# Kernel tuning notes

Measured on AMD Instinct MI355X. Metric: run time of the kernel, lower is better.

The kernel has to match this reference:

```python
import jax, jax.numpy as jnp
import numpy as np
from jax import lax

B, T_ENC, E = 32, 256, 512
A_RNN, D_RNN, P = 1024, 1024, 256
N_MEL, T_DEC = 80, 800
A_DIM, N_FILT, K = 128, 32, 31
PAD = (K - 1) // 2


def setup_inputs() -> dict:
    key = jax.random.key(0)
    ks = jax.random.split(key, 20)
    rn = lambda k, s, sc=0.02: jax.random.normal(k, s, dtype=jnp.float32) * sc
    return {
        "encoder_outputs": jax.random.normal(ks[0], (B, T_ENC, E), dtype=jnp.float32),
        "decoder_inputs": jax.random.normal(ks[1], (B, N_MEL, T_DEC), dtype=jnp.float32),
        "input_lengths": jax.random.randint(ks[2], (B,), 128, T_ENC + 1),
        "prenet_w1": rn(ks[3], (P, N_MEL)),
        "prenet_w2": rn(ks[4], (P, P)),
        "attn_rnn_Wih": rn(ks[5], (4 * A_RNN, P + E)),
        "attn_rnn_Whh": rn(ks[6], (4 * A_RNN, A_RNN)),
        "attn_rnn_bih": jnp.zeros((4 * A_RNN,), jnp.float32),
        "attn_rnn_bhh": jnp.zeros((4 * A_RNN,), jnp.float32),
        "query_W": rn(ks[7], (A_RNN, A_DIM)),
        "memory_W": rn(ks[8], (E, A_DIM)),
        "v_w": rn(ks[9], (A_DIM,)),
        "loc_conv_W": rn(ks[10], (N_FILT, 2, K)),
        "loc_lin_W": rn(ks[11], (N_FILT, A_DIM)),
        "dec_rnn_Wih": rn(ks[12], (4 * D_RNN, A_RNN + E)),
        "dec_rnn_Whh": rn(ks[13], (4 * D_RNN, D_RNN)),
        "dec_rnn_bih": jnp.zeros((4 * D_RNN,), jnp.float32),
        "dec_rnn_bhh": jnp.zeros((4 * D_RNN,), jnp.float32),
        "proj_W": rn(ks[14], (D_RNN + E, N_MEL)),
        "proj_b": jnp.zeros((N_MEL,), jnp.float32),
        "gate_W": rn(ks[15], (D_RNN + E, 1)),
        "gate_b": jnp.zeros((1,), jnp.float32),
    }


def _lstm_cell(xin, h0, c0, Wih, Whh, bih, bhh):
    # PyTorch LSTMCell gate order: i, f, g, o
    g = xin @ Wih.T + bih + h0 @ Whh.T + bhh
    i, f, gg, o = jnp.split(g, 4, axis=-1)
    c = jax.nn.sigmoid(f) * c0 + jax.nn.sigmoid(i) * jnp.tanh(gg)
    return jax.nn.sigmoid(o) * jnp.tanh(c), c


def _forward(encoder_outputs, decoder_inputs, prenet_w1, prenet_w2,
             attn_rnn_Wih, attn_rnn_Whh, attn_rnn_bih, attn_rnn_bhh,
             query_W, memory_W, v_w, loc_conv_W, loc_lin_W,
             dec_rnn_Wih, dec_rnn_Whh, dec_rnn_bih, dec_rnn_bhh,
             proj_W, proj_b, gate_W, gate_b, input_lengths):
    b, t_enc, e = encoder_outputs.shape
    n_mel = decoder_inputs.shape[1]
    dt = encoder_outputs.dtype

    # parse_decoder_inputs + go frame; keep the T_dec frames actually consumed
    x = jnp.transpose(decoder_inputs, (2, 0, 1))               # [T_dec, B, n_mel]
    go = jnp.zeros((1, b, n_mel), dt)
    x = jnp.concatenate([go, x], 0)[:-1]                       # [T_dec, B, n_mel]

    # Prenet: relu->dropout(p=0.5, always on) x2 (deterministic keys)
    k1, k2 = jax.random.split(jax.random.key(42))
    h = jax.nn.relu(jnp.einsum('tbm,pm->tbp', x, prenet_w1))
    h = h * jax.random.bernoulli(k1, 0.5, h.shape) * 2.0
    h = jax.nn.relu(jnp.einsum('tbp,qp->tbq', h, prenet_w2))
    pre = h * jax.random.bernoulli(k2, 0.5, h.shape) * 2.0     # [T_dec, B, P]

    valid = jnp.arange(t_enc)[None, :] < input_lengths[:, None]  # [B, T_enc]
    pmem = jnp.einsum('bte,ea->bta', encoder_outputs, memory_W)  # processed memory

    def step(carry, xstep):
        ah, ac, dh, dc, ctx, aw, awc = carry
        ah, ac = _lstm_cell(jnp.concatenate([xstep, ctx], -1), ah, ac,
                            attn_rnn_Wih, attn_rnn_Whh, attn_rnn_bih, attn_rnn_bhh)
        # location-sensitive attention (LSA)
        loc = jnp.stack([aw, awc], 1)                           # [B, 2, T_enc]
        lf = lax.conv_general_dilated(loc, loc_conv_W, (1,), [(PAD, PAD)],
                                      dimension_numbers=('NCH', 'OIH', 'NCH'))
        lf = jnp.einsum('bft,fa->bta', lf, loc_lin_W)           # [B, T_enc, A_DIM]
        q = ah @ query_W                                        # [B, A_DIM]
        energies = jnp.tanh(q[:, None, :] + lf + pmem) @ v_w    # [B, T_enc]
        energies = jnp.where(valid, energies, jnp.asarray(-1e9, dt))
        aw = jax.nn.softmax(energies, axis=-1)
        awc = awc + aw
        ctx = jnp.einsum('bt,bte->be', aw, encoder_outputs)
        dh, dc = _lstm_cell(jnp.concatenate([ah, ctx], -1), dh, dc,
                            dec_rnn_Wih, dec_rnn_Whh, dec_rnn_bih, dec_rnn_bhh)
        hc = jnp.concatenate([dh, ctx], -1)
        mel = hc @ proj_W + proj_b                              # [B, n_mel]
        gate = (hc @ gate_W + gate_b)[:, 0]                     # [B]
        return (ah, ac, dh, dc, ctx, aw, awc), (mel, gate, aw)

    z = lambda d: jnp.zeros((b, d), dt)
    carry0 = (z(A_RNN), z(A_RNN), z(D_RNN), z(D_RNN), z(e),
              jnp.zeros((b, t_enc), dt), jnp.zeros((b, t_enc), dt))
    _, (mels, gates, aligns) = lax.scan(step, carry0, pre)

    mel_outputs = jnp.transpose(mels, (1, 2, 0))                # [B, n_mel, T_dec]
    gate_outputs = gates.T                                      # [B, T_dec]
    alignments = jnp.transpose(aligns, (1, 0, 2))               # [B, T_dec, T_enc]
    return mel_outputs, gate_outputs, alignments


def reference(encoder_outputs, decoder_inputs, input_lengths, prenet_w1, prenet_w2,
              attn_rnn_Wih, attn_rnn_Whh, attn_rnn_bih, attn_rnn_bhh,
              query_W, memory_W, v_w, loc_conv_W, loc_lin_W,
              dec_rnn_Wih, dec_rnn_Whh, dec_rnn_bih, dec_rnn_bhh,
              proj_W, proj_b, gate_W, gate_b):
    return _forward(encoder_outputs, decoder_inputs, prenet_w1, prenet_w2,
                    attn_rnn_Wih, attn_rnn_Whh, attn_rnn_bih, attn_rnn_bhh,
                    query_W, memory_W, v_w, loc_conv_W, loc_lin_W,
                    dec_rnn_Wih, dec_rnn_Whh, dec_rnn_bih, dec_rnn_bhh,
                    proj_W, proj_b, gate_W, gate_b, input_lengths)
```

## Files before the change

### kernel.cpp

```cpp
#include <hip/hip_runtime.h>
#include <hip/hip_cooperative_groups.h>
#include <cstdint>
#include <cstddef>
#include <cstring>

constexpr int TDEC   = 800;

constexpr int AH_OFF   = 0;
constexpr int AC_OFF   = 65536;
constexpr int DH_OFF   = 98304;
constexpr int DC_OFF   = 163840;
constexpr int CTX_OFF  = 196608;
constexpr int AW_OFF   = 229376;
constexpr int AWC_OFF  = 237568;
constexpr int BAR_OFF  = 245760;
constexpr int STATE_FLOATS = 253952;
constexpr int PRE_OFF  = 253952;
constexpr int PMEM_OFF = 6807552;
constexpr int W1T_OFF  = 7856128;
constexpr int W2T_OFF  = 7876608;
constexpr int LINT_OFF = 7942144;
constexpr int BLOB_OFF = 7946240;
constexpr int WCHUNKS_A = 14;
constexpr int WCHUNKS_D = 20;
constexpr int WBLK_DW  = 34816;

constexpr int SCRATCH_F     = 5376;
constexpr int SMEM_BYTES    = 139264 + SCRATCH_F * 4;

typedef __attribute__((ext_vector_type(4))) float f32x4;
typedef __attribute__((ext_vector_type(4))) unsigned int u32x4;

__device__ __forceinline__ void coh_load4(const float* p, f32x4& v) {
  asm volatile("global_load_dwordx4 %0, %1, off sc0 sc1" : "=v"(v) : "v"(p));
}
__device__ __forceinline__ void coh_load1(const float* p, float& v) {
  asm volatile("global_load_dword %0, %1, off sc0 sc1" : "=v"(v) : "v"(p));
}
__device__ __forceinline__ void coh_store1(float* p, float v) {
  asm volatile("global_store_dword %0, %1, off sc0 sc1" :: "v"(p), "v"(v) : "memory");
}
__device__ __forceinline__ void coh_wait() {
  asm volatile("s_waitcnt vmcnt(0)" ::: "memory");
  __builtin_amdgcn_sched_barrier(0);
}

__device__ __forceinline__ void gbar(uint32_t* slots, uint32_t val) {
  asm volatile("s_waitcnt vmcnt(0)" ::: "memory");
  __syncthreads();
  if (threadIdx.x == 0) {
    uint32_t* p = slots + blockIdx.x;
    asm volatile("global_store_dword %0, %1, off sc0 sc1" :: "v"(p), "v"(val) : "memory");
  }
  if (threadIdx.x < 64) {
    const uint32_t* sp = slots + threadIdx.x * 4;
    while (true) {
      u32x4 v4;
      asm volatile("global_load_dwordx4 %0, %1, off sc0 sc1" : "=v"(v4) : "v"(sp) : "memory");
      asm volatile("s_waitcnt vmcnt(0)" ::: "memory");
      if (v4.x >= val && v4.y >= val && v4.z >= val && v4.w >= val) break;
      __builtin_amdgcn_s_sleep(2);
    }
  }
  __syncthreads();
}

__host__ __device__ inline void tf2x32(uint32_t k0, uint32_t k1, uint32_t& x0, uint32_t& x1) {
  const uint32_t ks2 = k0 ^ k1 ^ 0x1BD11BDAu;
  uint32_t y0 = x0 + k0, y1 = x1 + k1;
#define TFR(r) { y0 += y1; y1 = (y1 << (r)) | (y1 >> (32 - (r))); y1 ^= y0; }
  TFR(13) TFR(15) TFR(26) TFR(6)   y0 += k1;  y1 += ks2 + 1u;
  TFR(17) TFR(29) TFR(16) TFR(24)  y0 += ks2; y1 += k0 + 2u;
  TFR(13) TFR(15) TFR(26) TFR(6)   y0 += k0;  y1 += k1 + 3u;
  TFR(17) TFR(29) TFR(16) TFR(24)  y0 += k1;  y1 += ks2 + 4u;
  TFR(13) TFR(15) TFR(26) TFR(6)   y0 += ks2; y1 += k0 + 5u;
#undef TFR
  x0 = y0; x1 = y1;
}

__device__ inline bool tf_keep(uint32_t ka, uint32_t kb, uint32_t i) {
  uint32_t x0 = 0u, x1 = i;
  tf2x32(ka, kb, x0, x1);
  return (((x0 ^ x1) >> 31) == 0u);
}

__device__ inline float sigm(float x) { return 1.f / (1.f + expf(-x)); }

__device__ __forceinline__ const float* wsrc(int c, int j, int kk,
                                             const float* aWih, const float* aWhh,
                                             const float* dWih, const float* dWhh) {
  if (c < WCHUNKS_A) {
    int k = c * 128 + kk;
    return (k < 768) ? (aWih + (size_t)j * 768 + k)
                     : (aWhh + (size_t)j * 1024 + (k - 768));
  } else {
    int k = (c - WCHUNKS_A) * 128 + kk;
    return (k < 1536) ? (dWih + (size_t)j * 1536 + k)
                      : (dWhh + (size_t)j * 1024 + (k - 1536));
  }
}

__global__ __launch_bounds__(256) void transpose_k(const float* __restrict__ src,
                                                   float* __restrict__ dst, int R, int C) {
  int i = blockIdx.x * 256 + threadIdx.x;
  if (i < R * C) { int r = i / C, c = i % C; dst[c * R + r] = src[i]; }
}

__global__ __launch_bounds__(256) void prenet1_kernel(const float* __restrict__ decin,
                                                      const float* __restrict__ w1T,
                                                      float* __restrict__ pre,
                                                      uint32_t ka, uint32_t kb) {
  __shared__ float xs[32][81];
  const int t = blockIdx.x, tid = threadIdx.x;
  for (int f = tid; f < 32 * 80; f += 256) {
    int b = f / 80, m = f % 80;
    xs[b][m] = (t == 0) ? 0.f : decin[b * 64000 + m * 800 + (t - 1)];
  }
  __syncthreads();
  const int p = tid;
  float acc[32];
#pragma unroll
  for (int r = 0; r < 32; ++r) acc[r] = 0.f;
  for (int m = 0; m < 80; ++m) {
    float wv = w1T[m * 256 + p];
#pragma unroll
    for (int r = 0; r < 32; ++r) acc[r] += xs[r][m] * wv;
  }
  float* rowbase = pre + (size_t)t * 32 * 256;
#pragma unroll
  for (int r = 0; r < 32; ++r) {
    float v = fmaxf(acc[r], 0.f);
    uint32_t i = (uint32_t)((t * 32 + r) * 256 + p);
    rowbase[r * 256 + p] = tf_keep(ka, kb, i) ? v * 2.f : 0.f;
  }
}

__global__ __launch_bounds__(256) void prenet2_kernel(const float* __restrict__ w2T,
                                                      float* __restrict__ pre,
                                                      uint32_t ka, uint32_t kb) {
  __shared__ float hs[32][257];
  const int t = blockIdx.x, tid = threadIdx.x;
  float* rowbase = pre + (size_t)t * 32 * 256;
  for (int f = tid; f < 32 * 256; f += 256) {
    int b = f >> 8, k = f & 255;
    hs[b][k] = rowbase[b * 256 + k];
  }
  __syncthreads();
  const int p = tid;
  float acc[32];
#pragma unroll
  for (int r = 0; r < 32; ++r) acc[r] = 0.f;
  for (int k = 0; k < 256; ++k) {
    float wv = w2T[k * 256 + p];
#pragma unroll
    for (int r = 0; r < 32; ++r) acc[r] += hs[r][k] * wv;
  }
#pragma unroll
  for (int r = 0; r < 32; ++r) {
    float v = fmaxf(acc[r], 0.f);
    uint32_t i = (uint32_t)((t * 32 + r) * 256 + p);
    rowbase[r * 256 + p] = tf_keep(ka, kb, i) ? v * 2.f : 0.f;
  }
}

__global__ __launch_bounds__(128) void pmem_kernel(const float* __restrict__ enc,
                                                   const float* __restrict__ memW,
                                                   float* __restrict__ pmem) {
  __shared__ float es[8][513];
  const int b = blockIdx.x >> 5, tg = blockIdx.x & 31, t0 = tg * 8;
  const int tid = threadIdx.x;
  for (int f = tid; f < 8 * 512; f += 128) {
    int rr = f >> 9, e = f & 511;
    es[rr][e] = enc[(size_t)(b * 256 + t0 + rr) * 512 + e];
  }
  __syncthreads();
  float acc[8];
#pragma unroll
  for (int r = 0; r < 8; ++r) acc[r] = 0.f;
  const int a = tid;
  for (int e = 0; e < 512; ++e) {
    float wv = memW[e * 128 + a];
#pragma unroll
    for (int r = 0; r < 8; ++r) acc[r] += es[r][e] * wv;
  }
#pragma unroll
  for (int r = 0; r < 8; ++r) pmem[(size_t)(b * 256 + t0 + r) * 128 + a] = acc[r];
}

__global__ __launch_bounds__(1024) void mklo_kernel(const float* __restrict__ aWih,
                                                    const float* __restrict__ aWhh,
                                                    const float* __restrict__ dWih,
                                                    const float* __restrict__ dWhh,
                                                    uint32_t* __restrict__ blob) {
  __shared__ float tmp[2048];
  const int blk = blockIdx.x, tid = threadIdx.x;
  uint32_t* bdst = blob + (size_t)blk * WBLK_DW;
  for (int c = 0; c < WCHUNKS_A + WCHUNKS_D; ++c) {
    const int row16 = tid >> 6;
    const int kk = (tid & 63) * 2;
    const int j = (row16 >> 2) * 1024 + blk * 4 + (row16 & 3);
    float2 wv = *(const float2*)wsrc(c, j, kk, aWih, aWhh, dWih, dWhh);
    *(float2*)(tmp + row16 * 128 + kk) = wv;
    __syncthreads();
    const int rr = tid & 3, jgq = (tid >> 2) & 3, l = tid >> 4;
    uint32_t b0 = __float_as_uint(tmp[(jgq * 4 + rr) * 128 + l * 2]) & 0xffffu;
    uint32_t b1 = __float_as_uint(tmp[(jgq * 4 + rr) * 128 + l * 2 + 1]) & 0xffffu;
    bdst[c * 1024 + (l * 4 + jgq) * 4 + rr] = b0 | (b1 << 16);
    __syncthreads();
  }
}

struct ScanParams {
  const float* enc; const int* lens;
  const float* aWih; const float* aWhh; const float* abih; const float* abhh;
  const float* qW;   const float* vw;   const float* locW; const float* linT;
  const float* dWih; const float* dWhh; const float* dbih; const float* dbhh;
  const float* pW;   const float* pb;   const float* gW;   const float* gb;
  float* ah; float* ac; float* dh; float* dc; float* ctx; float* aw; float* awc;
  uint32_t* bar; const uint32_t* wlo;
  const float* pre; const float* pmem;
  float* mel_out; float* gate_out; float* align_out;
};

struct XW { const float* x; int ldx; int coh; };

template <typename F>
__device__ __forceinline__ void lstm_lds(int blk, int tid, int nc, F getx,
                                         const uint32_t* wch0, const uint32_t* lch0,
                                         const float* bih, const float* bhh,
                                         float* hout, float* cst,
                                         float* xs, float* gate_s) {
  const int lane = tid & 63;
  const int bg = (tid >> 6) & 3;
  const int jg = tid >> 8;
  const int b0 = bg * 8;
  const int hb = blk << 2;
  const int woff = (lane * 4 + jg) << 2;

  float acc[4][8];
#pragma unroll
  for (int rr = 0; rr < 4; ++rr) {
    float bv = (lane == 0) ? (bih[jg * 1024 + hb + rr] + bhh[jg * 1024 + hb + rr]) : 0.f;
#pragma unroll
    for (int bb = 0; bb < 8; ++bb) acc[rr][bb] = bv;
  }

  const int sb = tid >> 5;
  const int skq = (tid & 31) * 4;
  f32x4 sreg;
  u32x4 lcur, lnxt;
  {
    XW x0 = getx(0);
    const float* p = x0.x + (size_t)sb * x0.ldx + skq;
    lcur = *(const u32x4*)(lch0 + woff);
    if (x0.coh) { coh_load4(p, sreg); coh_wait(); }
    else        sreg = *(const f32x4*)p;
    *(f32x4*)(xs + sb * 132 + skq) = sreg;
  }
  __syncthreads();

  for (int c = 0; c < nc; ++c) {
    const bool more = (c + 1 < nc);
    if (more) {
      XW xn = getx(c + 1);
      const float* p = xn.x + (size_t)sb * xn.ldx + skq;
      lnxt = *(const u32x4*)(lch0 + (c + 1) * 1024 + woff);
      if (xn.coh) coh_load4(p, sreg);
      else        sreg = *(const f32x4*)p;
    }
    u32x4 wv = *(const u32x4*)(wch0 + c * 1024 + woff);
    float we[4], wo[4];
#pragma unroll
    for (int rr = 0; rr < 4; ++rr) {
      uint32_t h = wv[rr], l = lcur[rr];
      we[rr] = __uint_as_float((h << 16) | (l & 0xffffu));
      wo[rr] = __uint_as_float((h & 0xffff0000u) | (l >> 16));
    }
#pragma unroll
    for (int bb = 0; bb < 8; ++bb) {
      float2 x2 = *(const float2*)(xs + (b0 + bb) * 132 + lane * 2);
#pragma unroll
      for (int rr = 0; rr < 4; ++rr)
        acc[rr][bb] = fmaf(wo[rr], x2.y, fmaf(we[rr], x2.x, acc[rr][bb]));
    }
    __syncthreads();
    if (more) {
      coh_wait();
      *(f32x4*)(xs + sb * 132 + skq) = sreg;
      lcur = lnxt;
      __syncthreads();
    }
  }

  float v[32];
#pragma unroll
  for (int rr = 0; rr < 4; ++rr)
#pragma unroll
    for (int bb = 0; bb < 8; ++bb) v[rr * 8 + bb] = acc[rr][bb];
#pragma unroll
  for (int s = 0; s < 5; ++s) {
    const int d = 32 >> s;
    const int half = 32 >> (s + 1);
    const bool up = (lane & d) != 0;
#pragma unroll
    for (int i = 0; i < 16; ++i) {
      if (i < half) {
        float send = up ? v[i] : v[i + half];
        float got = __shfl_xor(send, d);
        v[i] = (up ? v[i + half] : v[i]) + got;
      }
    }
  }
  v[0] += __shfl_xor(v[0], 1);
  if ((lane & 1) == 0) {
    int p = (lane >> 1) & 31;
    int rr = p >> 3, bb = p & 7;
    gate_s[(jg * 4 + rr) * 33 + (b0 + bb)] = v[0];
  }
  __syncthreads();
  if (tid < 128) {
    int hl = tid >> 5, b = tid & 31;
    float gi = gate_s[(0 + hl) * 33 + b];
    float gf = gate_s[(4 + hl) * 33 + b];
    float gg = gate_s[(8 + hl) * 33 + b];
    float go = gate_s[(12 + hl) * 33 + b];
    int idx = b * 1024 + hb + hl;
    float c0v = cst[idx];
    float cn = sigm(gf) * c0v + sigm(gi) * tanhf(gg);
    cst[idx] = cn;
    coh_store1(hout + idx, sigm(go) * tanhf(cn));
  }
  __syncthreads();
}

__device__ void stage_attn(int b, int tid, int t, const ScanParams& P,
                           const float* ah_cur, float* ctx_out, float* S) {
  float* ah_l = S;
  float* part = S + 1024;
  float* lf   = S;
  float* sLoc = S + 4224;
  float* q_s  = S + 4800;
  float* vw_s = S + 4928;
  float* red  = S + 5056;
  float* aw_s = S + 5064;
  float* cpart= S + 1024;

  float ahv;
  coh_load1(ah_cur + b * 1024 + tid, ahv);
  if (tid < 572) {
    int c = tid / 286, i = tid % 286;
    int src = i - 15;
    float vv = 0.f;
    if (src >= 0 && src < 256) vv = (c == 0 ? P.aw : P.awc)[b * 256 + src];
    sLoc[c * 286 + i] = vv;
  } else if (tid < 700) {
    vw_s[tid - 572] = P.vw[tid - 572];
  }
  coh_wait();
  ah_l[tid] = ahv;
  __syncthreads();
  {
    const int js = tid >> 7, a = tid & 127;
    const float* ahb = ah_l + js * 128;
    const float* qp = P.qW + (size_t)(js * 128) * 128 + a;
    float p0 = 0.f, p1 = 0.f, p2 = 0.f, p3 = 0.f;
    for (int j = 0; j < 128; j += 4) {
      p0 += ahb[j] * qp[(size_t)j * 128];
      p1 += ahb[j + 1] * qp[(size_t)(j + 1) * 128];
      p2 += ahb[j + 2] * qp[(size_t)(j + 2) * 128];
      p3 += ahb[j + 3] * qp[(size_t)(j + 3) * 128];
    }
    part[tid] = (p0 + p1) + (p2 + p3);
  }
  __syncthreads();
  if (tid < 128) {
    float q = 0.f;
#pragma unroll
    for (int js = 0; js < 8; ++js) q += part[js * 128 + tid];
    q_s[tid] = q;
  }
  __syncthreads();
  const int len_b = P.lens[b];
#pragma unroll 1
  for (int h = 0; h < 2; ++h) {
    const int tt0 = h << 7;
    {
      const int f = tid >> 5, seg = tid & 31;
      float a0 = 0.f, a1 = 0.f, a2 = 0.f, a3 = 0.f;
      const float* wf = P.locW + f * 62;
#pragma unroll
      for (int c2 = 0; c2 < 2; ++c2)
#pragma unroll
        for (int k = 0; k < 31; ++k) {
          float wv = wf[c2 * 31 + k];
          const float* sl = sLoc + c2 * 286 + tt0 + seg * 4 + k;
          a0 = fmaf(sl[0], wv, a0); a1 = fmaf(sl[1], wv, a1);
          a2 = fmaf(sl[2], wv, a2); a3 = fmaf(sl[3], wv, a3);
        }
      lf[(seg * 4 + 0) * 33 + f] = a0; lf[(seg * 4 + 1) * 33 + f] = a1;
      lf[(seg * 4 + 2) * 33 + f] = a2; lf[(seg * 4 + 3) * 33 + f] = a3;
    }
    __syncthreads();
    {
      const int ttl = tid >> 3, aq = tid & 7;
      const int tt = tt0 + ttl;
      const float* pm = P.pmem + (size_t)(b * 256 + tt) * 128;
      const float* lfr = lf + ttl * 33;
      float lfv[32];
#pragma unroll
      for (int f = 0; f < 32; ++f) lfv[f] = lfr[f];
      float ep = 0.f;
#pragma unroll 2
      for (int ai = 0; ai < 16; ++ai) {
        int a = aq * 16 + ai;
        const float4* lt = (const float4*)(P.linT + a * 32);
        float lfa = 0.f;
#pragma unroll
        for (int u = 0; u < 8; ++u) {
          float4 l4 = lt[u];
          lfa += l4.x * lfv[u * 4] + l4.y * lfv[u * 4 + 1] + l4.z * lfv[u * 4 + 2] + l4.w * lfv[u * 4 + 3];
        }
        ep += vw_s[a] * tanhf(q_s[a] + lfa + pm[a]);
      }
      ep += __shfl_xor(ep, 1); ep += __shfl_xor(ep, 2); ep += __shfl_xor(ep, 4);
      if (aq == 0) aw_s[tt] = (tt < len_b) ? ep : -1e9f;
    }
    __syncthreads();
  }
  if (tid < 64) {
    float m0 = fmaxf(fmaxf(aw_s[tid], aw_s[64 + tid]), fmaxf(aw_s[128 + tid], aw_s[192 + tid]));
#pragma unroll
    for (int m = 32; m >= 1; m >>= 1) m0 = fmaxf(m0, __shfl_xor(m0, m));
    if (tid == 0) red[0] = m0;
  }
  __syncthreads();
  const float mx = red[0];
  if (tid < 256) aw_s[tid] = expf(aw_s[tid] - mx);
  __syncthreads();
  if (tid < 64) {
    float s0 = aw_s[tid] + aw_s[64 + tid] + aw_s[128 + tid] + aw_s[192 + tid];
#pragma unroll
    for (int m = 32; m >= 1; m >>= 1) s0 += __shfl_xor(s0, m);
    if (tid == 0) red[1] = s0;
  }
  __syncthreads();
  const float inv = 1.f / red[1];
  if (tid < 256) {
    float awv = aw_s[tid] * inv;
    aw_s[tid] = awv;
    P.aw[b * 256 + tid] = awv;
    P.awc[b * 256 + tid] += awv;
    P.align_out[(size_t)b * 204800 + (size_t)t * 256 + tid] = awv;
  }
  __syncthreads();
  {
    const int ee = tid & 511, hf = tid >> 9;
    const float* encb = P.enc + (size_t)b * 131072 + (size_t)hf * 128 * 512 + ee;
    float a0 = 0.f, a1 = 0.f, a2 = 0.f, a3 = 0.f;
    for (int tt = 0; tt < 128; tt += 4) {
      a0 += aw_s[hf * 128 + tt] * encb[(size_t)tt * 512];
      a1 += aw_s[hf * 128 + tt + 1] * encb[(size_t)(tt + 1) * 512];
      a2 += aw_s[hf * 128 + tt + 2] * encb[(size_t)(tt + 2) * 512];
      a3 += aw_s[hf * 128 + tt + 3] * encb[(size_t)(tt + 3) * 512];
    }
    cpart[hf * 512 + ee] = (a0 + a1) + (a2 + a3);
  }
  __syncthreads();
  if (tid < 512) coh_store1(ctx_out + b * 512 + tid, cpart[tid] + cpart[512 + tid]);
}

__device__ void stage_proj(int b, int tid, int tp, const ScanParams& P,
                           const float* dh_prev, const float* ctx_prev, float* S) {
  float* hc    = S;
  float* partm = S + 1536;
  float* partg = S + 2016;
  for (int i = tid; i < 1536; i += 1024) {
    float v;
    const float* p = (i < 1024) ? (dh_prev + b * 1024 + i) : (ctx_prev + b * 512 + (i - 1024));
    coh_load1(p, v);
    coh_wait();
    hc[i] = v;
  }
  __syncthreads();
  if (tid < 480) {
    int ks = tid / 80, m = tid % 80;
    const float* pWk = P.pW + (size_t)(ks * 256) * 80 + m;
    const float* hck = hc + ks * 256;
    float a0 = 0.f, a1 = 0.f, a2 = 0.f, a3 = 0.f;
    for (int k = 0; k < 256; k += 4) {
      a0 += hck[k] * pWk[(size_t)k * 80];
      a1 += hck[k + 1] * pWk[(size_t)(k + 1) * 80];
      a2 += hck[k + 2] * pWk[(size_t)(k + 2) * 80];
      a3 += hck[k + 3] * pWk[(size_t)(k + 3) * 80];
    }
    partm[ks * 80 + m] = (a0 + a1) + (a2 + a3);
  } else if (tid < 512) {
    int s = tid - 480;
    float acc = 0.f;
    for (int k = s * 48; k < s * 48 + 48; ++k) acc += hc[k] * P.gW[k];
    partg[s] = acc;
  }
  __syncthreads();
  if (tid < 80) {
    float acc = P.pb[tid];
#pragma unroll
    for (int s = 0; s < 6; ++s) acc += partm[s * 80 + tid];
    P.mel_out[b * 64000 + tid * 800 + tp] = acc;
  }
  if (tid == 511) {
    float acc = P.gb[0];
#pragma unroll
    for (int s = 0; s < 32; ++s) acc += partg[s];
    P.gate_out[b * 800 + tp] = acc;
  }
  __syncthreads();
}

__global__ void __launch_bounds__(1024, 4) scan_kernel(ScanParams P) {
  extern __shared__ char dynsmem[];
  uint32_t* wlds = (uint32_t*)dynsmem;
  float* scratch = (float*)(dynsmem + 139264);
  float* xs = scratch;
  float* gate_s = scratch + 4224;
  const int blk = blockIdx.x, tid = threadIdx.x;

  {
    float* tmp = xs;
    for (int c = 0; c < WCHUNKS_A + WCHUNKS_D; ++c) {
      const int row16 = tid >> 6;
      const int kk = (tid & 63) * 2;
      const int j = (row16 >> 2) * 1024 + blk * 4 + (row16 & 3);
      float2 wv = *(const float2*)wsrc(c, j, kk, P.aWih, P.aWhh, P.dWih, P.dWhh);
      *(float2*)(tmp + row16 * 128 + kk) = wv;
      __syncthreads();
      const int rr = tid & 3, jgq = (tid >> 2) & 3, l = tid >> 4;
      uint32_t hi0 = __float_as_uint(tmp[(jgq * 4 + rr) * 128 + l * 2]) >> 16;
      uint32_t hi1 = __float_as_uint(tmp[(jgq * 4 + rr) * 128 + l * 2 + 1]) >> 16;
      wlds[c * 1024 + (l * 4 + jgq) * 4 + rr] = hi0 | (hi1 << 16);
      __syncthreads();
    }
  }
  __syncthreads();

  const uint32_t* lblk = P.wlo + (size_t)blk * WBLK_DW;
  uint32_t* slots = P.bar;
  uint32_t bk = 0;

  for (int i = 0; i <= TDEC; ++i) {
    const int pi = i & 1, pim1 = pi ^ 1;
    if (i < TDEC) {
      const float* pre_t = P.pre + (size_t)i * 8192;
      const float* ctx_r = P.ctx + pim1 * 16384;
      const float* ah_r  = P.ah + pim1 * 32768;
      auto getxA = [&](int c) -> XW {
        XW r;
        if (c < 2)      { r.x = pre_t + c * 128;        r.ldx = 256;  r.coh = 0; }
        else if (c < 6) { r.x = ctx_r + (c - 2) * 128;  r.ldx = 512;  r.coh = 1; }
        else            { r.x = ah_r + (c - 6) * 128;   r.ldx = 1024; r.coh = 1; }
        return r;
      };
      lstm_lds(blk, tid, WCHUNKS_A, getxA, wlds, lblk, P.abih, P.abhh,
               P.ah + pi * 32768, P.ac, xs, gate_s);
    }
    if (i >= 1) {
      const float* ah_w  = P.ah + pim1 * 32768;
      const float* ctx_w = P.ctx + pim1 * 16384;
      const float* dh_r  = P.dh + pi * 32768;
      auto getxD = [&](int c) -> XW {
        XW r;
        if (c < 8)       { r.x = ah_w + c * 128;         r.ldx = 1024; r.coh = 1; }
        else if (c < 12) { r.x = ctx_w + (c - 8) * 128;  r.ldx = 512;  r.coh = 1; }
        else             { r.x = dh_r + (c - 12) * 128;  r.ldx = 1024; r.coh = 1; }
        return r;
      };
      lstm_lds(blk, tid, WCHUNKS_D, getxD, wlds + WCHUNKS_A * 1024,
               lblk + WCHUNKS_A * 1024, P.dbih, P.dbhh,
               P.dh + pim1 * 32768, P.dc, xs, gate_s);
    }
    gbar(slots, ++bk);
    if (blk < 32) {
      if (i < TDEC) stage_attn(blk, tid, i, P, P.ah + pi * 32768, P.ctx + pi * 16384, scratch);
    } else if (blk < 64) {
      if (i >= 1) stage_proj(blk - 32, tid, i - 1, P, P.dh + pim1 * 32768, P.ctx + pim1 * 16384, scratch);
    }
    gbar(slots, ++bk);
  }
}

extern "C" void kernel_launch(void* const* d_in, const int* in_sizes, int n_in,
                              void* d_out, int out_size, void* d_ws, size_t ws_size,
                              hipStream_t stream) {
  (void)in_sizes; (void)n_in; (void)out_size; (void)ws_size;
  const float* enc   = (const float*)d_in[0];
  const float* decin = (const float*)d_in[1];
  const int*   lens  = (const int*)d_in[2];
  const float* w1    = (const float*)d_in[3];
  const float* w2    = (const float*)d_in[4];
  const float* aWih  = (const float*)d_in[5];
  const float* aWhh  = (const float*)d_in[6];
  const float* abih  = (const float*)d_in[7];
  const float* abhh  = (const float*)d_in[8];
  const float* qW    = (const float*)d_in[9];
  const float* memW  = (const float*)d_in[10];
  const float* vw    = (const float*)d_in[11];
  const float* locW  = (const float*)d_in[12];
  const float* linW  = (const float*)d_in[13];
  const float* dWih  = (const float*)d_in[14];
  const float* dWhh  = (const float*)d_in[15];
  const float* dbih  = (const float*)d_in[16];
  const float* dbhh  = (const float*)d_in[17];
  const float* pW    = (const float*)d_in[18];
  const float* pb    = (const float*)d_in[19];
  const float* gW    = (const float*)d_in[20];
  const float* gb    = (const float*)d_in[21];

  float* ws  = (float*)d_ws;
  float* out = (float*)d_out;

  (void)hipMemsetAsync(ws, 0, (size_t)STATE_FLOATS * sizeof(float), stream);

  uint32_t k1a, k1b, k2a, k2b;
  { uint32_t a = 0u, b = 0u; tf2x32(0u, 42u, a, b); k1a = a; k1b = b; }
  { uint32_t a = 0u, b = 1u; tf2x32(0u, 42u, a, b); k2a = a; k2b = b; }

  transpose_k<<<dim3((256 * 80 + 255) / 256), dim3(256), 0, stream>>>(w1, ws + W1T_OFF, 256, 80);
  transpose_k<<<dim3((256 * 256 + 255) / 256), dim3(256), 0, stream>>>(w2, ws + W2T_OFF, 256, 256);
  transpose_k<<<dim3((32 * 128 + 255) / 256), dim3(256), 0, stream>>>(linW, ws + LINT_OFF, 32, 128);
  prenet1_kernel<<<dim3(800), dim3(256), 0, stream>>>(decin, ws + W1T_OFF, ws + PRE_OFF, k1a, k1b);
  prenet2_kernel<<<dim3(800), dim3(256), 0, stream>>>(ws + W2T_OFF, ws + PRE_OFF, k2a, k2b);
  pmem_kernel<<<dim3(1024), dim3(128), 0, stream>>>(enc, memW, ws + PMEM_OFF);
  mklo_kernel<<<dim3(256), dim3(1024), 0, stream>>>(aWih, aWhh, dWih, dWhh,
                                                    (uint32_t*)(ws + BLOB_OFF));

  ScanParams prm;
  prm.enc = enc; prm.lens = lens;
  prm.aWih = aWih; prm.aWhh = aWhh; prm.abih = abih; prm.abhh = abhh;
  prm.qW = qW; prm.vw = vw; prm.locW = locW; prm.linT = ws + LINT_OFF;
  prm.dWih = dWih; prm.dWhh = dWhh; prm.dbih = dbih; prm.dbhh = dbhh;
  prm.pW = pW; prm.pb = pb; prm.gW = gW; prm.gb = gb;
  prm.ah = ws + AH_OFF; prm.ac = ws + AC_OFF;
  prm.dh = ws + DH_OFF; prm.dc = ws + DC_OFF;
  prm.ctx = ws + CTX_OFF; prm.aw = ws + AW_OFF; prm.awc = ws + AWC_OFF;
  prm.bar = (uint32_t*)(ws + BAR_OFF);
  prm.wlo = (const uint32_t*)(ws + BLOB_OFF);
  prm.pre = ws + PRE_OFF; prm.pmem = ws + PMEM_OFF;
  prm.mel_out = out; prm.gate_out = out + 2048000; prm.align_out = out + 2073600;

  (void)hipFuncSetAttribute((const void*)scan_kernel,
                            hipFuncAttributeMaxDynamicSharedMemorySize, SMEM_BYTES);

  void* kargs[] = { (void*)&prm };
  (void)hipLaunchCooperativeKernel(scan_kernel, dim3(256), dim3(1024), kargs, SMEM_BYTES, stream);
}
```

Measured before the change: 391.7 ms.

## Replace coherent loads with acquire fence at barrier; relayout packed weights

```diff
diff --git a/kernel.cpp b/kernel.cpp
--- a/kernel.cpp
+++ b/kernel.cpp
@@ -31,18 +31,8 @@
 typedef __attribute__((ext_vector_type(4))) float f32x4;
 typedef __attribute__((ext_vector_type(4))) unsigned int u32x4;
 
-__device__ __forceinline__ void coh_load4(const float* p, f32x4& v) {
-  asm volatile("global_load_dwordx4 %0, %1, off sc0 sc1" : "=v"(v) : "v"(p));
-}
-__device__ __forceinline__ void coh_load1(const float* p, float& v) {
-  asm volatile("global_load_dword %0, %1, off sc0 sc1" : "=v"(v) : "v"(p));
-}
 __device__ __forceinline__ void coh_store1(float* p, float v) {
   asm volatile("global_store_dword %0, %1, off sc0 sc1" :: "v"(p), "v"(v) : "memory");
-}
-__device__ __forceinline__ void coh_wait() {
-  asm volatile("s_waitcnt vmcnt(0)" ::: "memory");
-  __builtin_amdgcn_sched_barrier(0);
 }
 
 __device__ __forceinline__ void gbar(uint32_t* slots, uint32_t val) {
@@ -63,6 +53,7 @@
     }
   }
   __syncthreads();
+  __builtin_amdgcn_fence(__ATOMIC_ACQUIRE, "agent");
 }
 
 __host__ __device__ inline void tf2x32(uint32_t k0, uint32_t k1, uint32_t& x0, uint32_t& x1) {
@@ -205,7 +196,7 @@
     const int rr = tid & 3, jgq = (tid >> 2) & 3, l = tid >> 4;
     uint32_t b0 = __float_as_uint(tmp[(jgq * 4 + rr) * 128 + l * 2]) & 0xffffu;
     uint32_t b1 = __float_as_uint(tmp[(jgq * 4 + rr) * 128 + l * 2 + 1]) & 0xffffu;
-    bdst[c * 1024 + (l * 4 + jgq) * 4 + rr] = b0 | (b1 << 16);
+    bdst[c * 1024 + jgq * 256 + l * 4 + rr] = b0 | (b1 << 16);
     __syncthreads();
   }
 }
@@ -222,7 +213,7 @@
   float* mel_out; float* gate_out; float* align_out;
 };
 
-struct XW { const float* x; int ldx; int coh; };
+struct XW { const float* x; int ldx; };
 
 template <typename F>
 __device__ __forceinline__ void lstm_lds(int blk, int tid, int nc, F getx,
@@ -235,7 +226,7 @@
   const int jg = tid >> 8;
   const int b0 = bg * 8;
   const int hb = blk << 2;
-  const int woff = (lane * 4 + jg) << 2;
+  const int woff = jg * 256 + lane * 4;
 
   float acc[4][8];
 #pragma unroll
@@ -251,10 +242,8 @@
   u32x4 lcur, lnxt;
   {
     XW x0 = getx(0);
-    const float* p = x0.x + (size_t)sb * x0.ldx + skq;
     lcur = *(const u32x4*)(lch0 + woff);
-    if (x0.coh) { coh_load4(p, sreg); coh_wait(); }
-    else        sreg = *(const f32x4*)p;
+    sreg = *(const f32x4*)(x0.x + (size_t)sb * x0.ldx + skq);
     *(f32x4*)(xs + sb * 132 + skq) = sreg;
   }
   __syncthreads();
@@ -263,10 +252,8 @@
     const bool more = (c + 1 < nc);
     if (more) {
       XW xn = getx(c + 1);
-      const float* p = xn.x + (size_t)sb * xn.ldx + skq;
       lnxt = *(const u32x4*)(lch0 + (c + 1) * 1024 + woff);
-      if (xn.coh) coh_load4(p, sreg);
-      else        sreg = *(const f32x4*)p;
+      sreg = *(const f32x4*)(xn.x + (size_t)sb * xn.ldx + skq);
     }
     u32x4 wv = *(const u32x4*)(wch0 + c * 1024 + woff);
     float we[4], wo[4];
@@ -285,7 +272,6 @@
     }
     __syncthreads();
     if (more) {
-      coh_wait();
       *(f32x4*)(xs + sb * 132 + skq) = sreg;
       lcur = lnxt;
       __syncthreads();
@@ -327,7 +313,7 @@
     int idx = b * 1024 + hb + hl;
     float c0v = cst[idx];
     float cn = sigm(gf) * c0v + sigm(gi) * tanhf(gg);
-    cst[idx] = cn;
+    coh_store1(cst + idx, cn);
     coh_store1(hout + idx, sigm(go) * tanhf(cn));
   }
   __syncthreads();
@@ -345,8 +331,7 @@
   float* aw_s = S + 5064;
   float* cpart= S + 1024;
 
-  float ahv;
-  coh_load1(ah_cur + b * 1024 + tid, ahv);
+  float ahv = ah_cur[b * 1024 + tid];
   if (tid < 572) {
     int c = tid / 286, i = tid % 286;
     int src = i - 15;
@@ -356,7 +341,6 @@
   } else if (tid < 700) {
     vw_s[tid - 572] = P.vw[tid - 572];
   }
-  coh_wait();
   ah_l[tid] = ahv;
   __syncthreads();
   {
@@ -448,9 +432,9 @@
   if (tid < 256) {
     float awv = aw_s[tid] * inv;
     aw_s[tid] = awv;
-    P.aw[b * 256 + tid] = awv;
-    P.awc[b * 256 + tid] += awv;
-    P.align_out[(size_t)b * 204800 + (size_t)t * 256 + tid] = awv;
+    coh_store1(P.aw + b * 256 + tid, awv);
+    coh_store1(P.awc + b * 256 + tid, P.awc[b * 256 + tid] + awv);
+    coh_store1(P.align_out + (size_t)b * 204800 + (size_t)t * 256 + tid, awv);
   }
   __syncthreads();
   {
@@ -474,13 +458,8 @@
   float* hc    = S;
   float* partm = S + 1536;
   float* partg = S + 2016;
-  for (int i = tid; i < 1536; i += 1024) {
-    float v;
-    const float* p = (i < 1024) ? (dh_prev + b * 1024 + i) : (ctx_prev + b * 512 + (i - 1024));
-    coh_load1(p, v);
-    coh_wait();
-    hc[i] = v;
-  }
+  for (int i = tid; i < 1536; i += 1024)
+    hc[i] = (i < 1024) ? dh_prev[b * 1024 + i] : ctx_prev[b * 512 + (i - 1024)];
   __syncthreads();
   if (tid < 480) {
     int ks = tid / 80, m = tid % 80;
@@ -505,13 +484,13 @@
     float acc = P.pb[tid];
 #pragma unroll
     for (int s = 0; s < 6; ++s) acc += partm[s * 80 + tid];
-    P.mel_out[b * 64000 + tid * 800 + tp] = acc;
+    coh_store1(P.mel_out + b * 64000 + tid * 800 + tp, acc);
   }
   if (tid == 511) {
     float acc = P.gb[0];
 #pragma unroll
     for (int s = 0; s < 32; ++s) acc += partg[s];
-    P.gate_out[b * 800 + tp] = acc;
+    coh_store1(P.gate_out + b * 800 + tp, acc);
   }
   __syncthreads();
 }
@@ -536,7 +515,7 @@
       const int rr = tid & 3, jgq = (tid >> 2) & 3, l = tid >> 4;
       uint32_t hi0 = __float_as_uint(tmp[(jgq * 4 + rr) * 128 + l * 2]) >> 16;
       uint32_t hi1 = __float_as_uint(tmp[(jgq * 4 + rr) * 128 + l * 2 + 1]) >> 16;
-      wlds[c * 1024 + (l * 4 + jgq) * 4 + rr] = hi0 | (hi1 << 16);
+      wlds[c * 1024 + jgq * 256 + l * 4 + rr] = hi0 | (hi1 << 16);
       __syncthreads();
     }
   }
@@ -554,9 +533,9 @@
       const float* ah_r  = P.ah + pim1 * 32768;
       auto getxA = [&](int c) -> XW {
         XW r;
-        if (c < 2)      { r.x = pre_t + c * 128;        r.ldx = 256;  r.coh = 0; }
-        else if (c < 6) { r.x = ctx_r + (c - 2) * 128;  r.ldx = 512;  r.coh = 1; }
-        else            { r.x = ah_r + (c - 6) * 128;   r.ldx = 1024; r.coh = 1; }
+        if (c < 2)      { r.x = pre_t + c * 128;        r.ldx = 256;  }
+        else if (c < 6) { r.x = ctx_r + (c - 2) * 128;  r.ldx = 512;  }
+        else            { r.x = ah_r + (c - 6) * 128;   r.ldx = 1024; }
         return r;
       };
       lstm_lds(blk, tid, WCHUNKS_A, getxA, wlds, lblk, P.abih, P.abhh,
@@ -568,9 +547,9 @@
       const float* dh_r  = P.dh + pi * 32768;
       auto getxD = [&](int c) -> XW {
         XW r;
-        if (c < 8)       { r.x = ah_w + c * 128;         r.ldx = 1024; r.coh = 1; }
-        else if (c < 12) { r.x = ctx_w + (c - 8) * 128;  r.ldx = 512;  r.coh = 1; }
-        else             { r.x = dh_r + (c - 12) * 128;  r.ldx = 1024; r.coh = 1; }
+        if (c < 8)       { r.x = ah_w + c * 128;         r.ldx = 1024; }
+        else if (c < 12) { r.x = ctx_w + (c - 8) * 128;  r.ldx = 512;  }
+        else             { r.x = dh_r + (c - 12) * 128;  r.ldx = 1024; }
         return r;
       };
       lstm_lds(blk, tid, WCHUNKS_D, getxD, wlds + WCHUNKS_A * 1024,
```

After: 374.1 ms. 1.05x faster.
